# Performance work log

Hardware: AMD Instinct MI355X
Metric: run time of the kernel (lower is better)

## Reference

```python
import jax, jax.numpy as jnp
import numpy as np
from jax import lax

B, T_DEC, T_ENC = 32, 400, 300
N_MEL, PRENET, ENC_D = 80, 256, 512
ATT_RNN, DEC_RNN, ATT_D = 512, 512, 128
LOC_F, LOC_K = 32, 31


def setup_inputs() -> dict:
    key = jax.random.key(0)
    ks = jax.random.split(key, 24)

    def w(k, shape):
        return jax.random.normal(k, shape, jnp.float32) / np.float32(np.sqrt(shape[-1]))

    inp = {
        "encoder_out": jax.random.normal(ks[0], (B, T_ENC, ENC_D), jnp.float32),
        "mels": jax.random.normal(ks[1], (B, T_DEC, N_MEL), jnp.float32),
        "lengths": jax.random.randint(ks[2], (B,), 1, T_ENC + 1).astype(jnp.int32),
        # prenet (3 layers, no bias)
        "W_p0": w(ks[3], (PRENET, N_MEL)),
        "W_p1": w(ks[4], (PRENET, PRENET)),
        "W_p2": w(ks[5], (PRENET, PRENET)),
        # attention GRUCell: input = prenet_dim + enc_dim = 768
        "W_ih_a": w(ks[6], (3 * ATT_RNN, PRENET + ENC_D)),
        "W_hh_a": w(ks[7], (3 * ATT_RNN, ATT_RNN)),
        "b_ih_a": jnp.zeros((3 * ATT_RNN,), jnp.float32),
        "b_hh_a": jnp.zeros((3 * ATT_RNN,), jnp.float32),
        # decoder GRUCell: input = attn_rnn + enc_dim = 1024 (what the code actually feeds)
        "W_ih_d": w(ks[8], (3 * DEC_RNN, ATT_RNN + ENC_D)),
        "W_hh_d": w(ks[9], (3 * DEC_RNN, DEC_RNN)),
        "b_ih_d": jnp.zeros((3 * DEC_RNN,), jnp.float32),
        "b_hh_d": jnp.zeros((3 * DEC_RNN,), jnp.float32),
        # location-sensitive attention
        "W_q": w(ks[10], (ATT_D, ATT_RNN)),
        "W_m": w(ks[11], (ATT_D, ENC_D)),
        "K_loc": w(ks[12], (LOC_F, 2, LOC_K)),
        "W_l": w(ks[13], (ATT_D, LOC_F)),
        "v": w(ks[14], (ATT_D,)),
        # output projection + gate
        "W_out": w(ks[15], (N_MEL, DEC_RNN + ENC_D)),
        "b_out": jnp.zeros((N_MEL,), jnp.float32),
        "W_g": w(ks[16], (1, DEC_RNN + ENC_D)),
        "b_g": jnp.zeros((1,), jnp.float32),
    }
    return inp


def _gru_cell(x, h, W_ih, W_hh, b_ih, b_hh):
    gi = x @ W_ih.T + b_ih
    gh = h @ W_hh.T + b_hh
    i_r, i_z, i_n = jnp.split(gi, 3, axis=-1)
    h_r, h_z, h_n = jnp.split(gh, 3, axis=-1)
    r = jax.nn.sigmoid(i_r + h_r)
    z = jax.nn.sigmoid(i_z + h_z)
    n = jnp.tanh(i_n + r * h_n)
    return (1.0 - z) * n + z * h


def _decoder_core(encoder_out, mels, lengths, W_p0, W_p1, W_p2,
                  W_ih_a, W_hh_a, b_ih_a, b_hh_a, W_ih_d, W_hh_d, b_ih_d, b_hh_d,
                  W_q, W_m, K_loc, W_l, v, W_out, b_out, W_g, b_g):
    Bb, T_enc, _ = encoder_out.shape
    T_dec = mels.shape[1]
    pmem = encoder_out @ W_m.T  # [B,T_enc,ATT_D], computed once
    enc_mask = jnp.arange(T_enc)[None, :] < lengths[:, None]  # [B,T_enc]
    # shifted teacher-forcing inputs: zero first frame, then mels[:, :-1]
    dec_inputs = jnp.concatenate(
        [jnp.zeros((Bb, 1, mels.shape[2]), mels.dtype), mels[:, :-1]], axis=1)
    drop_key = jax.random.key(42)
    pad = LOC_K // 2

    def prenet(x, t):
        for i, W in enumerate((W_p0, W_p1, W_p2)):
            x = jax.nn.relu(x @ W.T)
            k = jax.random.fold_in(drop_key, t * 3 + i)
            keep = jax.random.bernoulli(k, 0.5, x.shape)
            x = jnp.where(keep, x * 2.0, 0.0)  # inverted dropout p=0.5 (hardcoded training=True)
        return x

    def step(carry, xs):
        ah, dh, ctx, aw, aw_sum = carry
        frame, t = xs
        x = prenet(frame, t)
        ah = _gru_cell(jnp.concatenate([x, ctx], -1), ah, W_ih_a, W_hh_a, b_ih_a, b_hh_a)
        # location features from current + cumulative attention weights
        awc = jnp.stack([aw, aw_sum], axis=1)  # [B,2,T_enc]
        loc = lax.conv_general_dilated(awc, K_loc, (1,), [(pad, pad)],
                                       dimension_numbers=("NCH", "OIH", "NCH"))
        loc = jnp.swapaxes(loc, 1, 2) @ W_l.T  # [B,T_enc,ATT_D]
        e = jnp.tanh((ah @ W_q.T)[:, None, :] + pmem + loc) @ v  # [B,T_enc]
        e = jnp.where(enc_mask, e, -1e9)
        aw_new = jax.nn.softmax(e, axis=-1)
        ctx = jnp.einsum("bt,btd->bd", aw_new, encoder_out)
        aw_sum = aw_sum + aw_new
        dh = _gru_cell(jnp.concatenate([ah, ctx], -1), dh, W_ih_d, W_hh_d, b_ih_d, b_hh_d)
        dhc = jnp.concatenate([dh, ctx], -1)
        mel = dhc @ W_out.T + b_out  # [B,N_MEL]
        gate = (dhc @ W_g.T + b_g)[:, 0]  # [B]
        return (ah, dh, ctx, aw_new, aw_sum), (mel, gate, aw_new)

    f32 = encoder_out.dtype
    init = (jnp.zeros((Bb, ATT_RNN), f32), jnp.zeros((Bb, DEC_RNN), f32),
            jnp.zeros((Bb, ENC_D), f32), jnp.zeros((Bb, T_enc), f32),
            jnp.zeros((Bb, T_enc), f32))
    frames = jnp.swapaxes(dec_inputs, 0, 1)  # [T_dec,B,N_MEL]
    _, (mels_out, gates, aligns) = lax.scan(jax.checkpoint(step), init,
                                            (frames, jnp.arange(T_dec)))
    mel_outputs = jnp.transpose(mels_out, (1, 2, 0))  # [B,N_MEL,T_dec]
    gate_outputs = jnp.swapaxes(gates, 0, 1)          # [B,T_dec]
    alignments = jnp.swapaxes(aligns, 0, 1)           # [B,T_dec,T_enc]
    return mel_outputs, gate_outputs, alignments


def reference(encoder_out, mels, lengths, W_p0, W_p1, W_p2,
              W_ih_a, W_hh_a, b_ih_a, b_hh_a, W_ih_d, W_hh_d, b_ih_d, b_hh_d,
              W_q, W_m, K_loc, W_l, v, W_out, b_out, W_g, b_g):
    return _decoder_core(encoder_out, mels, lengths, W_p0, W_p1, W_p2,
                         W_ih_a, W_hh_a, b_ih_a, b_hh_a, W_ih_d, W_hh_d, b_ih_d, b_hh_d,
                         W_q, W_m, K_loc, W_l, v, W_out, b_out, W_g, b_g)
```

## Files before the change

kernel.cpp:

```cpp
#include <hip/hip_runtime.h>
#include <cstdint>


static constexpr int TDEC = 400, TENC = 300, NMEL = 80;

__device__ __forceinline__ uint2 threefry2x32(uint32_t k0, uint32_t k1,
                                              uint32_t x0, uint32_t x1) {
  uint32_t k2 = k0 ^ k1 ^ 0x1BD11BDAu;
  x0 += k0; x1 += k1;
#define TFR(r) { x0 += x1; x1 = (x1 << (r)) | (x1 >> (32 - (r))); x1 ^= x0; }
  TFR(13) TFR(15) TFR(26) TFR(6)
  x0 += k1; x1 += k2 + 1u;
  TFR(17) TFR(29) TFR(16) TFR(24)
  x0 += k2; x1 += k0 + 2u;
  TFR(13) TFR(15) TFR(26) TFR(6)
  x0 += k0; x1 += k1 + 3u;
  TFR(17) TFR(29) TFR(16) TFR(24)
  x0 += k1; x1 += k2 + 4u;
  TFR(13) TFR(15) TFR(26) TFR(6)
  x0 += k2; x1 += k0 + 5u;
#undef TFR
  return make_uint2(x0, x1);
}

__device__ __forceinline__ bool keep_mask(uint32_t key0, uint32_t key1, uint32_t idx) {
  uint2 o = threefry2x32(key0, key1, 0u, idx);
  uint32_t bits = o.x ^ o.y;
  float u = __uint_as_float((bits >> 9) | 0x3f800000u) - 1.0f;
  return u < 0.5f;
}

__device__ __forceinline__ float dot4(float4 w, float4 a) {
  return w.x * a.x + w.y * a.y + w.z * a.z + w.w * a.w;
}
__device__ __forceinline__ float nt_load(const float* p) {
  return __builtin_nontemporal_load(p);
}

template <int K>
__device__ __forceinline__ void prenet_layer(const float* in_lds, float* out_lds,
                                             float* out_g, const float* __restrict__ W,
                                             uint32_t key0, uint32_t key1, int b0) {
  const int tid = threadIdx.x;
  const int cgp = tid & 63, bg = tid >> 6;
  float acc[4][4];
#pragma unroll
  for (int cc = 0; cc < 4; ++cc)
#pragma unroll
    for (int rr = 0; rr < 4; ++rr) acc[cc][rr] = 0.f;
  const float4* W4 = (const float4*)W;
  const float4* in4 = (const float4*)in_lds;
  for (int k4 = 0; k4 < K / 4; ++k4) {
    float4 a[4];
#pragma unroll
    for (int rr = 0; rr < 4; ++rr) a[rr] = in4[(bg * 4 + rr) * (K / 4) + k4];
#pragma unroll
    for (int cc = 0; cc < 4; ++cc) {
      float4 w = W4[(cgp + 64 * cc) * (K / 4) + k4];
#pragma unroll
      for (int rr = 0; rr < 4; ++rr) acc[cc][rr] += dot4(w, a[rr]);
    }
  }
#pragma unroll
  for (int cc = 0; cc < 4; ++cc)
#pragma unroll
    for (int rr = 0; rr < 4; ++rr) {
      int c = cgp + 64 * cc, br = bg * 4 + rr;
      float val = fmaxf(acc[cc][rr], 0.f);
      val = keep_mask(key0, key1, (uint32_t)((b0 + br) * 256 + c)) ? val * 2.f : 0.f;
      if (out_lds) out_lds[br * 256 + c] = val;
      if (out_g) out_g[(b0 + br) * 256 + c] = val;
    }
  __syncthreads();
}

__global__ __launch_bounds__(256) void prenet_kernel(const float* __restrict__ mels,
                                                     const float* __restrict__ Wp0,
                                                     const float* __restrict__ Wp1,
                                                     const float* __restrict__ Wp2,
                                                     float* __restrict__ x_all) {
  __shared__ float bufA[16 * 256];
  __shared__ float bufB[16 * 256];
  const int t = blockIdx.x >> 1, b0 = (blockIdx.x & 1) * 16;
  const int tid = threadIdx.x;
  for (int i = tid; i < 16 * 80; i += 256) {
    int br = i / 80, k = i % 80;
    bufB[br * 80 + k] = (t == 0) ? 0.f : mels[((b0 + br) * TDEC + (t - 1)) * NMEL + k];
  }
  __syncthreads();
  uint2 k0v = threefry2x32(0u, 42u, 0u, (uint32_t)(t * 3 + 0));
  uint2 k1v = threefry2x32(0u, 42u, 0u, (uint32_t)(t * 3 + 1));
  uint2 k2v = threefry2x32(0u, 42u, 0u, (uint32_t)(t * 3 + 2));
  prenet_layer<80>(bufB, bufA, nullptr, Wp0, k0v.x, k0v.y, b0);
  prenet_layer<256>(bufA, bufB, nullptr, Wp1, k1v.x, k1v.y, b0);
  prenet_layer<256>(bufB, nullptr, x_all + t * 8192, Wp2, k2v.x, k2v.y, b0);
}

__global__ __launch_bounds__(256) void pmem_kernel(const float* __restrict__ enc,
                                                   const float* __restrict__ Wm,
                                                   float* __restrict__ pmem) {
  const int b = blockIdx.x / 10, pc = blockIdx.x % 10;
  const int j = threadIdx.x & 127, ph = threadIdx.x >> 7;
  const float4* Wm4 = (const float4*)Wm;
  const float4* enc4 = (const float4*)enc + (size_t)(b * 300 + pc * 30 + ph * 15) * 128;
  float acc[15];
#pragma unroll
  for (int pp = 0; pp < 15; ++pp) acc[pp] = 0.f;
  for (int k4 = 0; k4 < 128; ++k4) {
    float4 w = Wm4[j * 128 + k4];
#pragma unroll
    for (int pp = 0; pp < 15; ++pp) acc[pp] += dot4(w, enc4[pp * 128 + k4]);
  }
#pragma unroll
  for (int pp = 0; pp < 15; ++pp)
    pmem[(size_t)(b * 300 + pc * 30 + ph * 15 + pp) * 128 + j] = acc[pp];
}

struct GP {
  const float *xall, *enc, *pmem;
  const int* lens;
  const float *Wiha, *Whha, *biha, *bhha;
  const float *Wihd, *Whhd, *bihd, *bhhd;
  const float *Wq, *Kloc, *Wl, *vv, *Wout, *bout, *Wg, *bg;
  float *ah, *dh, *ctx, *aw, *awsum, *e;
  float *omel, *ogate, *oalign;
};

template <int KIN>
__device__ __forceinline__ void gru_phase(const float4* __restrict__ A4, int a4n,
                                          const float4* __restrict__ B4,
                                          const float4* __restrict__ H4,
                                          const float* __restrict__ Wih,
                                          const float* __restrict__ Whh,
                                          const float* __restrict__ bih,
                                          const float* __restrict__ bhh,
                                          const float* __restrict__ hprev,
                                          float* __restrict__ hout,
                                          int idx0, float* lds) {
  const int tid = threadIdx.x;
  const int row = tid >> 3, seg = tid & 7;
  constexpr int K4I = KIN / 4;
  constexpr int SI = K4I / 8;
  const float4* Wih4 = (const float4*)Wih;
  const float4* Whh4 = (const float4*)Whh;
  float acc[24];
#pragma unroll
  for (int g = 0; g < 24; ++g) acc[g] = 0.f;
  for (int s = 0; s < SI; ++s) {
    int k4 = seg * SI + s;
    float4 a = (k4 < a4n) ? A4[row * a4n + k4] : B4[row * 128 + (k4 - a4n)];
#pragma unroll
    for (int gate = 0; gate < 3; ++gate)
#pragma unroll
      for (int i = 0; i < 4; ++i)
        acc[gate * 4 + i] += dot4(Wih4[(size_t)(gate * 512 + idx0 + i) * K4I + k4], a);
  }
  for (int s = 0; s < 16; ++s) {
    int k4 = seg * 16 + s;
    float4 a = H4[row * 128 + k4];
#pragma unroll
    for (int gate = 0; gate < 3; ++gate)
#pragma unroll
      for (int i = 0; i < 4; ++i)
        acc[12 + gate * 4 + i] += dot4(Whh4[(size_t)(gate * 512 + idx0 + i) * 128 + k4], a);
  }
#pragma unroll
  for (int g = 0; g < 24; ++g) lds[(g * 32 + row) * 8 + seg] = acc[g];
  __syncthreads();
  if (tid < 128) {
    int i = tid >> 5, r = tid & 31;
    float gi[3], gh[3];
#pragma unroll
    for (int gate = 0; gate < 3; ++gate) {
      float si = 0.f, sh = 0.f;
#pragma unroll
      for (int s = 0; s < 8; ++s) {
        si += lds[((gate * 4 + i) * 32 + r) * 8 + s];
        sh += lds[((12 + gate * 4 + i) * 32 + r) * 8 + s];
      }
      gi[gate] = si + bih[gate * 512 + idx0 + i];
      gh[gate] = sh + bhh[gate * 512 + idx0 + i];
    }
    float rr = 1.f / (1.f + expf(-(gi[0] + gh[0])));
    float zz = 1.f / (1.f + expf(-(gi[1] + gh[1])));
    float nn = tanhf(gi[2] + rr * gh[2]);
    float hp = hprev[r * 512 + idx0 + i];
    hout[r * 512 + idx0 + i] = (1.f - zz) * nn + zz * hp;
  }
}

__global__ __launch_bounds__(256) void k_gru(GP P, int t) {
  __shared__ float lds[6144];
  const int blk = blockIdx.x;
  const int p0 = t & 1, p1 = p0 ^ 1;
  if (blk < 128) {
    if (t < TDEC)
      gru_phase<768>((const float4*)(P.xall + (size_t)t * 8192), 64,
                     (const float4*)(P.ctx + p1 * 16384),
                     (const float4*)(P.ah + p1 * 16384),
                     P.Wiha, P.Whha, P.biha, P.bhha,
                     P.ah + p1 * 16384, P.ah + p0 * 16384, blk * 4, lds);
  } else {
    if (t >= 1)
      gru_phase<1024>((const float4*)(P.ah + p1 * 16384), 128,
                      (const float4*)(P.ctx + p1 * 16384),
                      (const float4*)(P.dh + p0 * 16384),
                      P.Wihd, P.Whhd, P.bihd, P.bhhd,
                      P.dh + p0 * 16384, P.dh + p1 * 16384, (blk - 128) * 4, lds);
  }
}

__global__ __launch_bounds__(256) void k_energy(GP P, int t) {
  __shared__ float smem[5056];
  const int tid = threadIdx.x;
  const int blk = blockIdx.x;
  const int p0 = t & 1, p1 = p0 ^ 1;

  if (blk >= 128) {
    if (t < 1) return;
    const int r = blk - 128;
    float* dhcx = smem;
    float* opl = smem + 1024;
    for (int i = tid; i < 512; i += 256) {
      dhcx[i] = P.dh[p1 * 16384 + r * 512 + i];
      dhcx[512 + i] = P.ctx[p1 * 16384 + r * 512 + i];
    }
    __syncthreads();
    if (tid < 162) {
      int m = tid >> 1, h = tid & 1;
      const float4* W4 = (m < 80) ? ((const float4*)P.Wout + (size_t)m * 256)
                                  : (const float4*)P.Wg;
      const float4* x4 = (const float4*)dhcx;
      float a = 0.f;
      for (int k4 = h * 128; k4 < h * 128 + 128; ++k4) a += dot4(W4[k4], x4[k4]);
      opl[tid] = a;
    }
    __syncthreads();
    if (tid < 81) {
      float sum = opl[tid * 2] + opl[tid * 2 + 1];
      if (tid < 80) P.omel[(size_t)(r * 80 + tid) * 400 + (t - 1)] = sum + P.bout[tid];
      else P.ogate[r * 400 + (t - 1)] = sum + P.bg[0];
    }
    return;
  }

  if (t >= TDEC) return;
  float* qp = smem;
  float* qb = smem + 256;
  float* awW = smem + 384;
  float* asW = smem + 496;
  float2* t2f = (float2*)(smem + 608);
  float* convl = smem + 2592;
  const int r = blk >> 2, q = blk & 3;
  const int pbase = q * 75;

  for (int i = tid; i < 992; i += 256) {
    int f = i / 31, k = i % 31;
    t2f[i] = make_float2(P.Kloc[f * 62 + k], P.Kloc[f * 62 + 31 + k]);
  }
  for (int i = tid; i < 105; i += 256) {
    int p = pbase - 15 + i;
    bool ok = (p >= 0 && p < TENC);
    awW[i] = ok ? P.aw[r * 300 + p] : 0.f;
    asW[i] = ok ? P.awsum[r * 300 + p] : 0.f;
  }
  {
    int j = tid & 127, kh = tid >> 7;
    const float4* Wq4 = (const float4*)P.Wq;
    const float4* a4 = (const float4*)(P.ah + p0 * 16384 + r * 512);
    float acc = 0.f;
    for (int k4 = kh * 64; k4 < kh * 64 + 64; ++k4) acc += dot4(Wq4[j * 128 + k4], a4[k4]);
    qp[j * 2 + kh] = acc;
  }
  __syncthreads();
  if (tid < 128) qb[tid] = qp[tid * 2] + qp[tid * 2 + 1];
  {
    int f = tid & 31, pl0 = tid >> 5;
    for (int pl = pl0; pl < 75; pl += 8) {
      float a = 0.f;
#pragma unroll
      for (int k = 0; k < 31; ++k) {
        float2 tv = t2f[f * 31 + k];
        a += awW[pl + k] * tv.x + asW[pl + k] * tv.y;
      }
      convl[f * 76 + pl] = a;
    }
  }
  __syncthreads();
  {
    int w = tid >> 6, lane = tid & 63;
    float wl0[32], wl1[32];
#pragma unroll
    for (int f = 0; f < 32; ++f) {
      wl0[f] = P.Wl[lane * 32 + f];
      wl1[f] = P.Wl[(lane + 64) * 32 + f];
    }
    float v0 = P.vv[lane], v1 = P.vv[lane + 64];
    float q0 = qb[lane], q1 = qb[lane + 64];
    int len = P.lens[r];
    for (int pl = w; pl < 75; pl += 4) {
      int p = pbase + pl;
      float a0 = 0.f, a1 = 0.f;
#pragma unroll
      for (int f = 0; f < 32; ++f) {
        float c = convl[f * 76 + pl];
        a0 += c * wl0[f];
        a1 += c * wl1[f];
      }
      float e0 = tanhf(q0 + P.pmem[((size_t)r * 300 + p) * 128 + lane] + a0) * v0;
      float e1 = tanhf(q1 + P.pmem[((size_t)r * 300 + p) * 128 + 64 + lane] + a1) * v1;
      float es = e0 + e1;
#pragma unroll
      for (int off = 32; off > 0; off >>= 1) es += __shfl_xor(es, off, 64);
      if (lane == 0) P.e[r * 304 + p] = (p < len) ? es : -1e9f;
    }
  }
}

__global__ __launch_bounds__(256) void k_ctx(GP P, int t) {
  __shared__ float smem[600];
  float* e_l = smem;
  float* red = smem + 304;
  float* cpart = smem + 320;
  const int tid = threadIdx.x;
  const int r = blockIdx.x >> 3, s8 = blockIdx.x & 7;
  const int p0 = t & 1;
  const int w = tid >> 6, lane = tid & 63;

  for (int i = tid; i < 300; i += 256) e_l[i] = P.e[r * 304 + i];
  if (tid < 4) e_l[300 + tid] = -3.4e38f;
  __syncthreads();

  float mx = -3.4e38f;
  for (int i = tid; i < 304; i += 256) mx = fmaxf(mx, e_l[i]);
#pragma unroll
  for (int off = 32; off > 0; off >>= 1) mx = fmaxf(mx, __shfl_xor(mx, off, 64));
  if (lane == 0) red[w] = mx;
  __syncthreads();
  mx = fmaxf(fmaxf(red[0], red[1]), fmaxf(red[2], red[3]));
  __syncthreads();
  float ls = 0.f;
  for (int i = tid; i < 300; i += 256) {
    float ex = expf(e_l[i] - mx);
    e_l[i] = ex;
    ls += ex;
  }
#pragma unroll
  for (int off = 32; off > 0; off >>= 1) ls += __shfl_xor(ls, off, 64);
  if (lane == 0) red[w] = ls;
  __syncthreads();
  float inv = 1.f / (red[0] + red[1] + red[2] + red[3]);
  for (int i = tid; i < 300; i += 256) {
    float a = e_l[i] * inv;
    e_l[i] = a;
    if (s8 == 0) {
      P.aw[r * 300 + i] = a;
      P.awsum[r * 300 + i] += a;
      P.oalign[((size_t)(r * 400 + t)) * 300 + i] = a;
    }
  }
  __syncthreads();

  {
    int j = tid & 63, pc = tid >> 6;
    float cp = 0.f;
    const float* eb = P.enc + ((size_t)r * 300) * 512 + s8 * 64 + j;
    for (int p = pc * 75; p < pc * 75 + 75; ++p)
      cp += e_l[p] * nt_load(eb + (size_t)p * 512);
    cpart[pc * 64 + j] = cp;
  }
  __syncthreads();
  if (tid < 64)
    P.ctx[p0 * 16384 + r * 512 + s8 * 64 + tid] =
        cpart[tid] + cpart[64 + tid] + cpart[128 + tid] + cpart[192 + tid];
}

extern "C" void kernel_launch(void* const* d_in, const int* in_sizes, int n_in,
                              void* d_out, int out_size, void* d_ws, size_t ws_size,
                              hipStream_t stream) {
  const float* enc = (const float*)d_in[0];
  const float* mels = (const float*)d_in[1];
  const int* lens = (const int*)d_in[2];
  const float* Wp0 = (const float*)d_in[3];
  const float* Wp1 = (const float*)d_in[4];
  const float* Wp2 = (const float*)d_in[5];

  float* ws = (float*)d_ws;
  float* x_all = ws;
  float* pmem = x_all + 3276800;
  float* ah = pmem + 1228800;
  float* dh = ah + 32768;
  float* ctx = dh + 32768;
  float* aw = ctx + 32768;
  float* awsum = aw + 9600;
  float* e = awsum + 9600;

  (void)hipMemsetAsync(ah, 0, (3 * 32768 + 9600 + 9600 + 9728) * sizeof(float), stream);

  prenet_kernel<<<800, 256, 0, stream>>>(mels, Wp0, Wp1, Wp2, x_all);
  pmem_kernel<<<320, 256, 0, stream>>>(enc, (const float*)d_in[15], pmem);

  float* omel = (float*)d_out;
  float* ogate = omel + 32 * 80 * 400;
  float* oalign = ogate + 32 * 400;

  GP P;
  P.xall = x_all; P.enc = enc; P.pmem = pmem; P.lens = lens;
  P.Wiha = (const float*)d_in[6]; P.Whha = (const float*)d_in[7];
  P.biha = (const float*)d_in[8]; P.bhha = (const float*)d_in[9];
  P.Wihd = (const float*)d_in[10]; P.Whhd = (const float*)d_in[11];
  P.bihd = (const float*)d_in[12]; P.bhhd = (const float*)d_in[13];
  P.Wq = (const float*)d_in[14]; P.Kloc = (const float*)d_in[16];
  P.Wl = (const float*)d_in[17]; P.vv = (const float*)d_in[18];
  P.Wout = (const float*)d_in[19]; P.bout = (const float*)d_in[20];
  P.Wg = (const float*)d_in[21]; P.bg = (const float*)d_in[22];
  P.ah = ah; P.dh = dh; P.ctx = ctx; P.aw = aw; P.awsum = awsum; P.e = e;
  P.omel = omel; P.ogate = ogate; P.oalign = oalign;

  for (int t = 0; t <= TDEC; ++t) {
    k_gru<<<256, 256, 0, stream>>>(P, t);
    k_energy<<<160, 256, 0, stream>>>(P, t);
    if (t < TDEC) k_ctx<<<256, 256, 0, stream>>>(P, t);
  }
}
```

Baseline: 45.76 ms.

## Fuse softmax and context into energy kernel via split-softmax partials

Drops the separate k_ctx kernel. Each energy block computes a local softmax (max, sum) and a partial context vector over its quarter of encoder positions. Consumers (k_gru and the output head) combine the four partials using flash-style rescaling, and the next energy step rebuilds the attention weights from stored energies. This removes one kernel launch per decoder step and a global synchronisation point. In exchange, every k_gru block redundantly recombines the full 32x512 context into shared memory, and alignment and cumulative-weight writes move one step later.

```diff
diff --git a/kernel.cpp b/kernel.cpp
--- a/kernel.cpp
+++ b/kernel.cpp
@@ -122,13 +122,17 @@
   const float *Wiha, *Whha, *biha, *bhha;
   const float *Wihd, *Whhd, *bihd, *bhhd;
   const float *Wq, *Kloc, *Wl, *vv, *Wout, *bout, *Wg, *bg;
-  float *ah, *dh, *ctx, *aw, *awsum, *e;
+  float *ah, *dh;
+  float *e2;
+  float *pM, *pS;
+  float *V;
+  float *awsum2;
   float *omel, *ogate, *oalign;
 };
 
 template <int KIN>
 __device__ __forceinline__ void gru_phase(const float4* __restrict__ A4, int a4n,
-                                          const float4* __restrict__ B4,
+                                          const float4* B4,
                                           const float4* __restrict__ H4,
                                           const float* __restrict__ Wih,
                                           const float* __restrict__ Whh,
@@ -191,19 +195,47 @@
 
 __global__ __launch_bounds__(256) void k_gru(GP P, int t) {
   __shared__ float lds[6144];
-  const int blk = blockIdx.x;
+  __shared__ float ctxS[16384];
+  __shared__ float wqL[128];
+  const int tid = threadIdx.x, blk = blockIdx.x;
   const int p0 = t & 1, p1 = p0 ^ 1;
+
+  if (t == 0) {
+    for (int i = tid; i < 16384; i += 256) ctxS[i] = 0.f;
+  } else {
+    if (tid < 128) {
+      int row = tid >> 2, q = tid & 3;
+      float m = -3.4e38f;
+#pragma unroll
+      for (int j = 0; j < 4; ++j) m = fmaxf(m, P.pM[p1 * 128 + row * 4 + j]);
+      float z = 0.f;
+#pragma unroll
+      for (int j = 0; j < 4; ++j)
+        z += P.pS[p1 * 128 + row * 4 + j] * expf(P.pM[p1 * 128 + row * 4 + j] - m);
+      wqL[tid] = expf(P.pM[p1 * 128 + row * 4 + q] - m) / z;
+    }
+    __syncthreads();
+    const float* Vb = P.V + (size_t)p1 * 65536;
+    for (int i = tid; i < 16384; i += 256) {
+      int row = i >> 9, c = i & 511;
+      const float* v = Vb + (size_t)(row * 4) * 512 + c;
+      ctxS[i] = v[0] * wqL[row * 4 + 0] + v[512] * wqL[row * 4 + 1] +
+                v[1024] * wqL[row * 4 + 2] + v[1536] * wqL[row * 4 + 3];
+    }
+  }
+  __syncthreads();
+
   if (blk < 128) {
     if (t < TDEC)
       gru_phase<768>((const float4*)(P.xall + (size_t)t * 8192), 64,
-                     (const float4*)(P.ctx + p1 * 16384),
+                     (const float4*)ctxS,
                      (const float4*)(P.ah + p1 * 16384),
                      P.Wiha, P.Whha, P.biha, P.bhha,
                      P.ah + p1 * 16384, P.ah + p0 * 16384, blk * 4, lds);
   } else {
     if (t >= 1)
       gru_phase<1024>((const float4*)(P.ah + p1 * 16384), 128,
-                      (const float4*)(P.ctx + p1 * 16384),
+                      (const float4*)ctxS,
                       (const float4*)(P.dh + p0 * 16384),
                       P.Wihd, P.Whhd, P.bihd, P.bhhd,
                       P.dh + p0 * 16384, P.dh + p1 * 16384, (blk - 128) * 4, lds);
@@ -211,9 +243,8 @@
 }
 
 __global__ __launch_bounds__(256) void k_energy(GP P, int t) {
-  __shared__ float smem[5056];
-  const int tid = threadIdx.x;
-  const int blk = blockIdx.x;
+  __shared__ float smem[5400];
+  const int tid = threadIdx.x, blk = blockIdx.x;
   const int p0 = t & 1, p1 = p0 ^ 1;
 
   if (blk >= 128) {
@@ -221,9 +252,21 @@
     const int r = blk - 128;
     float* dhcx = smem;
     float* opl = smem + 1024;
+    float M = -3.4e38f;
+#pragma unroll
+    for (int j = 0; j < 4; ++j) M = fmaxf(M, P.pM[p1 * 128 + r * 4 + j]);
+    float Z = 0.f;
+#pragma unroll
+    for (int j = 0; j < 4; ++j)
+      Z += P.pS[p1 * 128 + r * 4 + j] * expf(P.pM[p1 * 128 + r * 4 + j] - M);
+    float w0 = expf(P.pM[p1 * 128 + r * 4 + 0] - M) / Z;
+    float w1 = expf(P.pM[p1 * 128 + r * 4 + 1] - M) / Z;
+    float w2 = expf(P.pM[p1 * 128 + r * 4 + 2] - M) / Z;
+    float w3 = expf(P.pM[p1 * 128 + r * 4 + 3] - M) / Z;
+    const float* Vb = P.V + (size_t)p1 * 65536 + (size_t)(r * 4) * 512;
     for (int i = tid; i < 512; i += 256) {
       dhcx[i] = P.dh[p1 * 16384 + r * 512 + i];
-      dhcx[512 + i] = P.ctx[p1 * 16384 + r * 512 + i];
+      dhcx[512 + i] = Vb[i] * w0 + Vb[512 + i] * w1 + Vb[1024 + i] * w2 + Vb[1536 + i] * w3;
     }
     __syncthreads();
     if (tid < 162) {
@@ -244,25 +287,62 @@
     return;
   }
 
+  const int r = blk >> 2, q = blk & 3;
+  const int pb = q * 75;
+  float* awW = smem;
+  float* asW = smem + 108;
+  float2* t2f = (float2*)(smem + 216);
+  float* convl = smem + 2200;
+  float* qpL = smem + 4632;
+  float* qbL = smem + 4888;
+  float* el = smem + 5016;
+  float* eex = smem + 5096;
+
+  if (t >= 1) {
+    float M = -3.4e38f;
+#pragma unroll
+    for (int j = 0; j < 4; ++j) M = fmaxf(M, P.pM[p1 * 128 + r * 4 + j]);
+    float Z = 0.f;
+#pragma unroll
+    for (int j = 0; j < 4; ++j)
+      Z += P.pS[p1 * 128 + r * 4 + j] * expf(P.pM[p1 * 128 + r * 4 + j] - M);
+    float inv = 1.f / Z;
+    for (int i = tid; i < 105; i += 256) {
+      int p = pb - 15 + i;
+      float a = 0.f, s = 0.f;
+      if (p >= 0 && p < TENC) {
+        a = expf(P.e2[p1 * 9728 + r * 304 + p] - M) * inv;
+        s = P.awsum2[p1 * 9600 + r * 300 + p] + a;
+      }
+      awW[i] = a;
+      asW[i] = s;
+      if (p >= pb && p < pb + 75) {
+        P.awsum2[p0 * 9600 + r * 300 + p] = s;
+        P.oalign[((size_t)(r * 400 + (t - 1))) * 300 + p] = a;
+      }
+    }
+  } else {
+    for (int i = tid; i < 105; i += 256) { awW[i] = 0.f; asW[i] = 0.f; }
+  }
   if (t >= TDEC) return;
-  float* qp = smem;
-  float* qb = smem + 256;
-  float* awW = smem + 384;
-  float* asW = smem + 496;
-  float2* t2f = (float2*)(smem + 608);
-  float* convl = smem + 2592;
-  const int r = blk >> 2, q = blk & 3;
-  const int pbase = q * 75;
 
   for (int i = tid; i < 992; i += 256) {
     int f = i / 31, k = i % 31;
     t2f[i] = make_float2(P.Kloc[f * 62 + k], P.Kloc[f * 62 + 31 + k]);
   }
-  for (int i = tid; i < 105; i += 256) {
-    int p = pbase - 15 + i;
-    bool ok = (p >= 0 && p < TENC);
-    awW[i] = ok ? P.aw[r * 300 + p] : 0.f;
-    asW[i] = ok ? P.awsum[r * 300 + p] : 0.f;
+  __syncthreads();
+
+  {
+    int f = tid & 31, pl0 = tid >> 5;
+    for (int pl = pl0; pl < 75; pl += 8) {
+      float a = 0.f;
+#pragma unroll
+      for (int k = 0; k < 31; ++k) {
+        float2 tv = t2f[f * 31 + k];
+        a += awW[pl + k] * tv.x + asW[pl + k] * tv.y;
+      }
+      convl[f * 76 + pl] = a;
+    }
   }
   {
     int j = tid & 127, kh = tid >> 7;
@@ -270,22 +350,10 @@
     const float4* a4 = (const float4*)(P.ah + p0 * 16384 + r * 512);
     float acc = 0.f;
     for (int k4 = kh * 64; k4 < kh * 64 + 64; ++k4) acc += dot4(Wq4[j * 128 + k4], a4[k4]);
-    qp[j * 2 + kh] = acc;
-  }
-  __syncthreads();
-  if (tid < 128) qb[tid] = qp[tid * 2] + qp[tid * 2 + 1];
-  {
-    int f = tid & 31, pl0 = tid >> 5;
-    for (int pl = pl0; pl < 75; pl += 8) {
-      float a = 0.f;
-#pragma unroll
-      for (int k = 0; k < 31; ++k) {
-        float2 tv = t2f[f * 31 + k];
-        a += awW[pl + k] * tv.x + asW[pl + k] * tv.y;
-      }
-      convl[f * 76 + pl] = a;
-    }
-  }
+    qpL[j * 2 + kh] = acc;
+  }
+  __syncthreads();
+  if (tid < 128) qbL[tid] = qpL[tid * 2] + qpL[tid * 2 + 1];
   __syncthreads();
   {
     int w = tid >> 6, lane = tid & 63;
@@ -296,10 +364,10 @@
       wl1[f] = P.Wl[(lane + 64) * 32 + f];
     }
     float v0 = P.vv[lane], v1 = P.vv[lane + 64];
-    float q0 = qb[lane], q1 = qb[lane + 64];
+    float q0 = qbL[lane], q1 = qbL[64 + lane];
     int len = P.lens[r];
     for (int pl = w; pl < 75; pl += 4) {
-      int p = pbase + pl;
+      int p = pb + pl;
       float a0 = 0.f, a1 = 0.f;
 #pragma unroll
       for (int f = 0; f < 32; ++f) {
@@ -312,67 +380,45 @@
       float es = e0 + e1;
 #pragma unroll
       for (int off = 32; off > 0; off >>= 1) es += __shfl_xor(es, off, 64);
-      if (lane == 0) P.e[r * 304 + p] = (p < len) ? es : -1e9f;
-    }
-  }
-}
-
-__global__ __launch_bounds__(256) void k_ctx(GP P, int t) {
-  __shared__ float smem[600];
-  float* e_l = smem;
-  float* red = smem + 304;
-  float* cpart = smem + 320;
-  const int tid = threadIdx.x;
-  const int r = blockIdx.x >> 3, s8 = blockIdx.x & 7;
-  const int p0 = t & 1;
-  const int w = tid >> 6, lane = tid & 63;
-
-  for (int i = tid; i < 300; i += 256) e_l[i] = P.e[r * 304 + i];
-  if (tid < 4) e_l[300 + tid] = -3.4e38f;
-  __syncthreads();
-
-  float mx = -3.4e38f;
-  for (int i = tid; i < 304; i += 256) mx = fmaxf(mx, e_l[i]);
-#pragma unroll
-  for (int off = 32; off > 0; off >>= 1) mx = fmaxf(mx, __shfl_xor(mx, off, 64));
-  if (lane == 0) red[w] = mx;
-  __syncthreads();
-  mx = fmaxf(fmaxf(red[0], red[1]), fmaxf(red[2], red[3]));
-  __syncthreads();
-  float ls = 0.f;
-  for (int i = tid; i < 300; i += 256) {
-    float ex = expf(e_l[i] - mx);
-    e_l[i] = ex;
-    ls += ex;
-  }
-#pragma unroll
-  for (int off = 32; off > 0; off >>= 1) ls += __shfl_xor(ls, off, 64);
-  if (lane == 0) red[w] = ls;
-  __syncthreads();
-  float inv = 1.f / (red[0] + red[1] + red[2] + red[3]);
-  for (int i = tid; i < 300; i += 256) {
-    float a = e_l[i] * inv;
-    e_l[i] = a;
-    if (s8 == 0) {
-      P.aw[r * 300 + i] = a;
-      P.awsum[r * 300 + i] += a;
-      P.oalign[((size_t)(r * 400 + t)) * 300 + i] = a;
-    }
-  }
-  __syncthreads();
-
+      if (lane == 0) {
+        float ev = (p < len) ? es : -1e9f;
+        P.e2[p0 * 9728 + r * 304 + p] = ev;
+        el[pl] = ev;
+      }
+    }
+  }
+  __syncthreads();
+  if (tid < 64) {
+    int lane = tid;
+    float m = -3.4e38f;
+    for (int i = lane; i < 75; i += 64) m = fmaxf(m, el[i]);
+#pragma unroll
+    for (int off = 32; off > 0; off >>= 1) m = fmaxf(m, __shfl_xor(m, off, 64));
+    float s = 0.f;
+    for (int i = lane; i < 75; i += 64) {
+      float x = expf(el[i] - m);
+      eex[i] = x;
+      s += x;
+    }
+#pragma unroll
+    for (int off = 32; off > 0; off >>= 1) s += __shfl_xor(s, off, 64);
+    if (lane == 0) {
+      P.pM[p0 * 128 + r * 4 + q] = m;
+      P.pS[p0 * 128 + r * 4 + q] = s;
+    }
+  }
+  __syncthreads();
   {
-    int j = tid & 63, pc = tid >> 6;
-    float cp = 0.f;
-    const float* eb = P.enc + ((size_t)r * 300) * 512 + s8 * 64 + j;
-    for (int p = pc * 75; p < pc * 75 + 75; ++p)
-      cp += e_l[p] * nt_load(eb + (size_t)p * 512);
-    cpart[pc * 64 + j] = cp;
-  }
-  __syncthreads();
-  if (tid < 64)
-    P.ctx[p0 * 16384 + r * 512 + s8 * 64 + tid] =
-        cpart[tid] + cpart[64 + tid] + cpart[128 + tid] + cpart[192 + tid];
+    float* Vw = P.V + (size_t)p0 * 65536 + (size_t)(r * 4 + q) * 512;
+#pragma unroll
+    for (int cc = 0; cc < 2; ++cc) {
+      int c = tid + cc * 256;
+      float acc = 0.f;
+      const float* eb = P.enc + ((size_t)(r * 300 + pb)) * 512 + c;
+      for (int po = 0; po < 75; ++po) acc += eex[po] * nt_load(eb + (size_t)po * 512);
+      Vw[c] = acc;
+    }
+  }
 }
 
 extern "C" void kernel_launch(void* const* d_in, const int* in_sizes, int n_in,
@@ -390,12 +436,14 @@
   float* pmem = x_all + 3276800;
   float* ah = pmem + 1228800;
   float* dh = ah + 32768;
-  float* ctx = dh + 32768;
-  float* aw = ctx + 32768;
-  float* awsum = aw + 9600;
-  float* e = awsum + 9600;
-
-  (void)hipMemsetAsync(ah, 0, (3 * 32768 + 9600 + 9600 + 9728) * sizeof(float), stream);
+  float* e2 = dh + 32768;
+  float* pM = e2 + 19456;
+  float* pS = pM + 256;
+  float* V = pS + 256;
+  float* awsum2 = V + 131072;
+
+  (void)hipMemsetAsync(ah, 0, (32768 + 32768) * sizeof(float), stream);
+  (void)hipMemsetAsync(awsum2, 0, 19200 * sizeof(float), stream);
 
   prenet_kernel<<<800, 256, 0, stream>>>(mels, Wp0, Wp1, Wp2, x_all);
   pmem_kernel<<<320, 256, 0, stream>>>(enc, (const float*)d_in[15], pmem);
@@ -414,12 +462,12 @@
   P.Wl = (const float*)d_in[17]; P.vv = (const float*)d_in[18];
   P.Wout = (const float*)d_in[19]; P.bout = (const float*)d_in[20];
   P.Wg = (const float*)d_in[21]; P.bg = (const float*)d_in[22];
-  P.ah = ah; P.dh = dh; P.ctx = ctx; P.aw = aw; P.awsum = awsum; P.e = e;
+  P.ah = ah; P.dh = dh; P.e2 = e2; P.pM = pM; P.pS = pS; P.V = V;
+  P.awsum2 = awsum2;
   P.omel = omel; P.ogate = ogate; P.oalign = oalign;
 
   for (int t = 0; t <= TDEC; ++t) {
     k_gru<<<256, 256, 0, stream>>>(P, t);
     k_energy<<<160, 256, 0, stream>>>(P, t);
-    if (t < TDEC) k_ctx<<<256, 256, 0, stream>>>(P, t);
-  }
-}
+  }
+}
```

New measurement: 50.05 ms. +9.4%, slower.
